# Performance work log

Measured on AMD Instinct MI355X. Metric: run time of the kernel, lower is better.

Reference implementation:

```python
import jax, jax.numpy as jnp
import numpy as np

N_A, N_D = 16384, 16384
D_EV = 4096      # d_inEvents (= rows of H_M)
H_DIM = 512      # hidden_dim
H1 = 1024        # hidden_dim1
H3 = 1024        # hidden_dim3
D_M = 4096       # d_inM (reconstruction output dim)


def _mlp2(x, w1, b1, w2, b2):
    return jax.nn.relu(x @ w1 + b1) @ w2 + b2


def setup_inputs() -> dict:
    key = jax.random.key(0)
    ks = jax.random.split(key, 32)
    s_in = (2.0 / D_EV) ** 0.5
    s_h1 = (2.0 / H1) ** 0.5
    s_2h = (2.0 / (2 * H_DIM)) ** 0.5
    s_h3 = (2.0 / H3) ** 0.5
    d = {
        "H_A": jax.random.uniform(ks[0], (N_A, D_EV), jnp.float32),
        "H_D": jax.random.uniform(ks[1], (N_D, D_EV), jnp.float32),
        "H_M": jax.random.uniform(ks[2], (D_EV, D_EV), jnp.float32),
    }
    for i, nm in enumerate(["A", "D", "M"]):
        d[f"w{nm}1"] = jax.random.normal(ks[3 + 4 * i], (D_EV, H1), jnp.float32) * s_in
        d[f"b{nm}1"] = jnp.zeros((H1,), jnp.float32)
        d[f"w{nm}2"] = jax.random.normal(ks[4 + 4 * i], (H1, H_DIM), jnp.float32) * s_h1
        d[f"b{nm}2"] = jnp.zeros((H_DIM,), jnp.float32)
    for i, nm in enumerate(["EA", "ED"]):
        d[f"w{nm}1"] = jax.random.normal(ks[16 + 4 * i], (2 * H_DIM, H3), jnp.float32) * s_2h
        d[f"b{nm}1"] = jnp.zeros((H3,), jnp.float32)
        d[f"w{nm}2"] = jax.random.normal(ks[17 + 4 * i], (H3, D_M), jnp.float32) * s_h3
        d[f"b{nm}2"] = jnp.zeros((D_M,), jnp.float32)
    return d


def reference(H_A, H_D, H_M,
              wA1, bA1, wA2, bA2,
              wD1, bD1, wD2, bD2,
              wM1, bM1, wM2, bM2,
              wEA1, bEA1, wEA2, bEA2,
              wED1, bED1, wED2, bED2):
    # Encoder (the torch.eye matmul is an identity and is elided)
    H_mean_A = _mlp2(H_A, wA1, bA1, wA2, bA2)   # [N_A, H_DIM]
    H_mean_D = _mlp2(H_D, wD1, bD1, wD2, bD2)   # [N_D, H_DIM]
    H_mean_M = _mlp2(H_M, wM1, bM1, wM2, bM2)   # [D_EV, H_DIM]
    # Pooling: per-column loop in torch == single matmul H^T @ H_mean
    sum_A = H_A.T @ H_mean_A                    # [D_EV, H_DIM]
    sum_D = H_D.T @ H_mean_D                    # [D_EV, H_DIM]
    EventA = jnp.concatenate([H_mean_M, sum_A], axis=1)  # [D_EV, 2*H_DIM]
    EventD = jnp.concatenate([H_mean_M, sum_D], axis=1)
    reconstructA = _mlp2(EventA, wEA1, bEA1, wEA2, bEA2)  # [D_EV, D_M]
    reconstructD = _mlp2(EventD, wED1, bED1, wED2, bED2)
    return (reconstructA, reconstructD, H_mean_A, H_mean_D, H_mean_M)
```

## Files before the change

kernel.cpp:

```cpp
#include <hip/hip_runtime.h>
#include <cstdint>
#include <cstddef>


typedef unsigned short u16;
typedef unsigned int u32;
typedef __bf16 bf16_t;
typedef bf16_t bf16x8 __attribute__((ext_vector_type(8)));
typedef float f32x4 __attribute__((ext_vector_type(4)));
typedef u16 u16x4 __attribute__((ext_vector_type(4)));
typedef u16 u16x8 __attribute__((ext_vector_type(8)));

__device__ __forceinline__ u16 f2bf(float x) {
  u32 u = __builtin_bit_cast(u32, x);
  u += 0x7FFFu + ((u >> 16) & 1u);
  return (u16)(u >> 16);
}
__device__ __forceinline__ float bf2f(u16 h) {
  u32 u = ((u32)h) << 16;
  return __builtin_bit_cast(float, u);
}

#define AS1(p) ((__attribute__((address_space(1))) void*)(p))
#define AS3(p) ((__attribute__((address_space(3))) void*)(p))

__global__ void detect_kernel(const u32* __restrict__ p, int* __restrict__ flag) {
  if (threadIdx.x == 0 && blockIdx.x == 0) {
    int cnt = 0;
    for (int i = 0; i < 64; ++i) {
      u32 b = (p[i] >> 8) & 0xFFu;
      cnt += (b >= 0x3Au && b < 0x40u) ? 1 : 0;
    }
    *flag = (cnt >= 32) ? 1 : 0;
  }
}

__global__ void convert_kernel(const void* __restrict__ src, u16* __restrict__ dst,
                               long n, const int* __restrict__ fl) {
  long i = ((long)blockIdx.x * 256 + threadIdx.x) * 8;
  if (i >= n) return;
  u16x8 r;
  if (*fl) {
    r = *(const u16x8*)((const u16*)src + i);
  } else {
    const float* s = (const float*)src + i;
#pragma unroll
    for (int j = 0; j < 8; ++j) r[j] = f2bf(s[j]);
  }
  *(u16x8*)(dst + i) = r;
}

__global__ void tconv_kernel(const void* __restrict__ src, long soff, u16* __restrict__ dst,
                             int R, int C, const int* __restrict__ fl) {
  __shared__ u16 t[32][33];
  const int dt = *fl;
  const int tx = threadIdx.x & 31, ty = threadIdx.x >> 5;
  const long c0 = (long)blockIdx.x * 32, r0 = (long)blockIdx.y * 32;
#pragma unroll
  for (int r = 0; r < 4; ++r) {
    int rr = ty * 4 + r;
    long off = soff + (r0 + rr) * (long)C + c0 + tx;
    t[rr][tx] = dt ? ((const u16*)src)[off] : f2bf(((const float*)src)[off]);
  }
  __syncthreads();
#pragma unroll
  for (int r = 0; r < 4; ++r) {
    int rr = ty * 4 + r;
    dst[(c0 + rr) * (long)R + r0 + tx] = t[tx][rr];
  }
}

__global__ void reduce4_kernel(const float* __restrict__ s, long stride,
                               u16* __restrict__ dst, long ldd, long n) {
  long i = (long)blockIdx.x * 256 + threadIdx.x;
  if (i >= n) return;
  float v = s[i] + s[i + stride] + s[i + 2 * stride] + s[i + 3 * stride];
  dst[(i >> 9) * ldd + (i & 511)] = f2bf(v);
}

__global__ __launch_bounds__(256) void gemm_bt_kernel(
    const u16* __restrict__ A, long lda,
    const u16* __restrict__ Bt, long ldb,
    long K,
    const void* __restrict__ bias, int relu,
    void* __restrict__ outd, long odoff, long ldod,
    float* __restrict__ outw, long ldow, long ozstride,
    u16* __restrict__ outb, long ldob,
    u16* __restrict__ outb2, long ldob2,
    u16* __restrict__ outT, long ldT,
    const int* __restrict__ fl) {
  __shared__ u16 As[128 * 32];
  __shared__ u16 Bs[128 * 32];

  const int t = threadIdx.x;
  const int l = t & 63;
  const int w = t >> 6;
  const int wx = w & 1, wy = w >> 1;
  const long m0 = (long)blockIdx.y * 128;
  const long n0 = (long)blockIdx.x * 128;
  const int dt = *fl;

  const long koff = (long)blockIdx.z * K;
  A += koff;
  Bt += koff;
  if (outw) outw += (long)blockIdx.z * ozstride;

  const int srow = w * 16 + (l >> 2);
  const int scol = (l & 3) * 8;
  const int la = l & 15, lq = l >> 4;

  f32x4 acc[4][4];
  const f32x4 zero = {0.f, 0.f, 0.f, 0.f};
#pragma unroll
  for (int i = 0; i < 4; ++i)
#pragma unroll
    for (int j = 0; j < 4; ++j) acc[i][j] = zero;

  for (long k0 = 0; k0 < K; k0 += 32) {
#pragma unroll
    for (int r = 0; r < 2; ++r) {
      const u16* ga = A + (m0 + r * 64 + srow) * lda + k0 + scol;
      __builtin_amdgcn_global_load_lds(AS1(ga), AS3(As + (r * 64 + w * 16) * 32), 16, 0, 0);
      const u16* gb = Bt + (n0 + r * 64 + srow) * ldb + k0 + scol;
      __builtin_amdgcn_global_load_lds(AS1(gb), AS3(Bs + (r * 64 + w * 16) * 32), 16, 0, 0);
    }
    __syncthreads();

    bf16x8 af[4], bfr[4];
#pragma unroll
    for (int i = 0; i < 4; ++i) {
      af[i] = *(const bf16x8*)(As + (wy * 64 + i * 16 + la) * 32 + lq * 8);
      bfr[i] = *(const bf16x8*)(Bs + (wx * 64 + i * 16 + la) * 32 + lq * 8);
    }
#pragma unroll
    for (int i = 0; i < 4; ++i)
#pragma unroll
      for (int j = 0; j < 4; ++j)
        acc[i][j] = __builtin_amdgcn_mfma_f32_16x16x32_bf16(af[i], bfr[j], acc[i][j], 0, 0, 0);
    __syncthreads();
  }

  const long gr0 = m0 + wy * 64;
  const long gc0 = n0 + wx * 64;
#pragma unroll
  for (int i = 0; i < 4; ++i) {
#pragma unroll
    for (int j = 0; j < 4; ++j) {
      const long gc = gc0 + j * 16 + la;
      const long grb = gr0 + i * 16 + lq * 4;
      float bv = 0.f;
      if (bias) bv = dt ? bf2f(((const u16*)bias)[gc]) : ((const float*)bias)[gc];
      float vv[4];
#pragma unroll
      for (int p = 0; p < 4; ++p) {
        float x = acc[i][j][p] + bv;
        if (relu) x = x > 0.f ? x : 0.f;
        vv[p] = x;
      }
      if (outd) {
        if (dt) {
          u16* o = (u16*)outd + odoff;
#pragma unroll
          for (int p = 0; p < 4; ++p) o[(grb + p) * ldod + gc] = f2bf(vv[p]);
        } else {
          float* o = (float*)outd + odoff;
#pragma unroll
          for (int p = 0; p < 4; ++p) o[(grb + p) * ldod + gc] = vv[p];
        }
      }
      if (outw) {
#pragma unroll
        for (int p = 0; p < 4; ++p) outw[(grb + p) * ldow + gc] = vv[p];
      }
      if (outb) {
#pragma unroll
        for (int p = 0; p < 4; ++p) outb[(grb + p) * ldob + gc] = f2bf(vv[p]);
      }
      if (outb2) {
#pragma unroll
        for (int p = 0; p < 4; ++p) outb2[(grb + p) * ldob2 + gc] = f2bf(vv[p]);
      }
      if (outT) {
        u16x4 pk;
#pragma unroll
        for (int p = 0; p < 4; ++p) pk[p] = f2bf(vv[p]);
        *(u16x4*)(outT + gc * ldT + grb) = pk;
      }
    }
  }
}

static void gemm(hipStream_t st, const u16* A, long lda, const u16* Bt, long ldb,
                 long M, long N, long K, int zsplit,
                 const void* bias, int relu,
                 void* outd, long odoff, long ldod,
                 float* outw, long ldow, long ozstride,
                 u16* outb, long ldob, u16* outb2, long ldob2,
                 u16* outT, long ldT, const int* fl) {
  dim3 g((unsigned)(N / 128), (unsigned)(M / 128), (unsigned)zsplit);
  gemm_bt_kernel<<<g, 256, 0, st>>>(A, lda, Bt, ldb, K, bias, relu, outd, odoff, ldod,
                                    outw, ldow, ozstride, outb, ldob, outb2, ldob2,
                                    outT, ldT, fl);
}

static void tconv(hipStream_t st, const void* src, long soff, u16* dst, int R, int C,
                  const int* fl) {
  tconv_kernel<<<dim3((unsigned)(C / 32), (unsigned)(R / 32)), 256, 0, st>>>(src, soff, dst, R,
                                                                             C, fl);
}

static void conv(hipStream_t st, const void* src, u16* dst, long n, const int* fl) {
  convert_kernel<<<(unsigned)((n / 8 + 255) / 256), 256, 0, st>>>(src, dst, n, fl);
}

extern "C" void kernel_launch(void* const* d_in, const int* in_sizes, int n_in,
                              void* d_out, int out_size, void* d_ws, size_t ws_size,
                              hipStream_t stream) {
  (void)in_sizes; (void)n_in; (void)out_size; (void)ws_size;
  const long NA = 16384, DEV = 4096, H1n = 1024, HD = 512, DM = 4096;

  char* ws = (char*)d_ws;
  u16* BIG = (u16*)(ws + 0L);
  u16* H1B = (u16*)(ws + 134217728L);
  float* SUMS = (float*)(ws + 134217728L);
  u16* HMT = (u16*)(ws + 167772160L);
  u16* EVA = (u16*)(ws + 184549376L);
  u16* EVD = (u16*)(ws + 192937984L);
  u16* WT1 = (u16*)(ws + 201326592L);
  u16* WT2 = (u16*)(ws + 209715200L);
  int* FLAG = (int*)(ws + 218103808L);

  const void* H_A = d_in[0];
  const void* H_D = d_in[1];
  const void* H_M = d_in[2];
  const void *wA1 = d_in[3], *bA1 = d_in[4], *wA2 = d_in[5], *bA2 = d_in[6];
  const void *wD1 = d_in[7], *bD1 = d_in[8], *wD2 = d_in[9], *bD2 = d_in[10];
  const void *wM1 = d_in[11], *bM1 = d_in[12], *wM2 = d_in[13], *bM2 = d_in[14];
  const void *wEA1 = d_in[15], *bEA1 = d_in[16], *wEA2 = d_in[17], *bEA2 = d_in[18];
  const void *wED1 = d_in[19], *bED1 = d_in[20], *wED2 = d_in[21], *bED2 = d_in[22];

  const long O_RA = 0, O_RD = 16777216, O_HA = 33554432, O_HD = 41943040, O_HM = 50331648;

  detect_kernel<<<1, 64, 0, stream>>>((const u32*)H_A, FLAG);

  tconv(stream, wM1, 0, WT1, (int)DEV, (int)H1n, FLAG);
  tconv(stream, wM2, 0, WT2, (int)H1n, (int)HD, FLAG);
  conv(stream, H_M, BIG, DEV * DEV, FLAG);
  gemm(stream, BIG, DEV, WT1, DEV, DEV, H1n, DEV, 1, bM1, 1,
       nullptr, 0, 0, nullptr, 0, 0, H1B, H1n, nullptr, 0, nullptr, 0, FLAG);
  gemm(stream, H1B, H1n, WT2, H1n, DEV, HD, H1n, 1, bM2, 0,
       d_out, O_HM, HD, nullptr, 0, 0, EVA, 1024, EVD, 1024, nullptr, 0, FLAG);

  tconv(stream, wA1, 0, WT1, (int)DEV, (int)H1n, FLAG);
  tconv(stream, wA2, 0, WT2, (int)H1n, (int)HD, FLAG);
  conv(stream, H_A, BIG, NA * DEV, FLAG);
  gemm(stream, BIG, DEV, WT1, DEV, NA, H1n, DEV, 1, bA1, 1,
       nullptr, 0, 0, nullptr, 0, 0, H1B, H1n, nullptr, 0, nullptr, 0, FLAG);
  gemm(stream, H1B, H1n, WT2, H1n, NA, HD, H1n, 1, bA2, 0,
       d_out, O_HA, HD, nullptr, 0, 0, nullptr, 0, nullptr, 0, HMT, NA, FLAG);
  tconv(stream, H_A, 0, BIG, (int)NA, (int)DEV, FLAG);
  gemm(stream, BIG, NA, HMT, NA, DEV, HD, 4096, 4, nullptr, 0,
       nullptr, 0, 0, SUMS, HD, 2097152L, nullptr, 0, nullptr, 0, nullptr, 0, FLAG);
  reduce4_kernel<<<8192, 256, 0, stream>>>(SUMS, 2097152L, EVA + 512, 1024L, DEV * HD);

  tconv(stream, wEA1, 0, WT1, (int)H1n, (int)H1n, FLAG);
  tconv(stream, wEA2, 0, WT2, (int)H1n, (int)DM, FLAG);
  gemm(stream, EVA, 1024, WT1, H1n, DEV, H1n, H1n, 1, bEA1, 1,
       nullptr, 0, 0, nullptr, 0, 0, H1B, H1n, nullptr, 0, nullptr, 0, FLAG);
  gemm(stream, H1B, H1n, WT2, H1n, DEV, DM, H1n, 1, bEA2, 0,
       d_out, O_RA, DM, nullptr, 0, 0, nullptr, 0, nullptr, 0, nullptr, 0, FLAG);

  tconv(stream, wD1, 0, WT1, (int)DEV, (int)H1n, FLAG);
  tconv(stream, wD2, 0, WT2, (int)H1n, (int)HD, FLAG);
  conv(stream, H_D, BIG, NA * DEV, FLAG);
  gemm(stream, BIG, DEV, WT1, DEV, NA, H1n, DEV, 1, bD1, 1,
       nullptr, 0, 0, nullptr, 0, 0, H1B, H1n, nullptr, 0, nullptr, 0, FLAG);
  gemm(stream, H1B, H1n, WT2, H1n, NA, HD, H1n, 1, bD2, 0,
       d_out, O_HD, HD, nullptr, 0, 0, nullptr, 0, nullptr, 0, HMT, NA, FLAG);
  tconv(stream, H_D, 0, BIG, (int)NA, (int)DEV, FLAG);
  gemm(stream, BIG, NA, HMT, NA, DEV, HD, 4096, 4, nullptr, 0,
       nullptr, 0, 0, SUMS, HD, 2097152L, nullptr, 0, nullptr, 0, nullptr, 0, FLAG);
  reduce4_kernel<<<8192, 256, 0, stream>>>(SUMS, 2097152L, EVD + 512, 1024L, DEV * HD);

  tconv(stream, wED1, 0, WT1, (int)H1n, (int)H1n, FLAG);
  tconv(stream, wED2, 0, WT2, (int)H1n, (int)DM, FLAG);
  gemm(stream, EVD, 1024, WT1, H1n, DEV, H1n, H1n, 1, bED1, 1,
       nullptr, 0, 0, nullptr, 0, 0, H1B, H1n, nullptr, 0, nullptr, 0, FLAG);
  gemm(stream, H1B, H1n, WT2, H1n, DEV, DM, H1n, 1, bED2, 0,
       d_out, O_RD, DM, nullptr, 0, 0, nullptr, 0, nullptr, 0, nullptr, 0, FLAG);
}
```

Measured before the change: 2.228 ms.

## Add double-buffered 256x256 GEMM kernel and swizzle LDS layout

Adds a new 512-thread GEMM kernel with 256x256 tiles, a 64-wide K step and double-buffered LDS staging, so the next K tile loads while MFMAs run. It replaces the big encoder layer-1 GEMMs and the reconstruction layer-2 GEMMs. The existing 128x128 kernel also gets an XOR swizzle on its LDS write and read offsets to reduce bank conflicts. reduce4 gains optional bias/relu parameters, but they are unused here. The large tile uses 128KB of LDS and many accumulators per thread, which may limit occupancy.

```diff
diff --git a/kernel.cpp b/kernel.cpp
--- a/kernel.cpp
+++ b/kernel.cpp
@@ -71,11 +71,16 @@
 }
 
 __global__ void reduce4_kernel(const float* __restrict__ s, long stride,
-                               u16* __restrict__ dst, long ldd, long n) {
+                               u16* __restrict__ dst, long ldd, long n, int cl,
+                               const void* __restrict__ bias, int relu,
+                               const int* __restrict__ fl) {
   long i = (long)blockIdx.x * 256 + threadIdx.x;
   if (i >= n) return;
   float v = s[i] + s[i + stride] + s[i + 2 * stride] + s[i + 3 * stride];
-  dst[(i >> 9) * ldd + (i & 511)] = f2bf(v);
+  long col = i & ((1L << cl) - 1);
+  if (bias) v += (*fl) ? bf2f(((const u16*)bias)[col]) : ((const float*)bias)[col];
+  if (relu) v = v > 0.f ? v : 0.f;
+  dst[(i >> cl) * ldd + col] = f2bf(v);
 }
 
 __global__ __launch_bounds__(256) void gemm_bt_kernel(
@@ -106,8 +111,9 @@
   if (outw) outw += (long)blockIdx.z * ozstride;
 
   const int srow = w * 16 + (l >> 2);
-  const int scol = (l & 3) * 8;
+  const int scol = (((l & 3) ^ ((l >> 2) & 3))) * 8;
   const int la = l & 15, lq = l >> 4;
+  const int fsl = (lq ^ (la & 3)) * 8;
 
   f32x4 acc[4][4];
   const f32x4 zero = {0.f, 0.f, 0.f, 0.f};
@@ -129,8 +135,8 @@
     bf16x8 af[4], bfr[4];
 #pragma unroll
     for (int i = 0; i < 4; ++i) {
-      af[i] = *(const bf16x8*)(As + (wy * 64 + i * 16 + la) * 32 + lq * 8);
-      bfr[i] = *(const bf16x8*)(Bs + (wx * 64 + i * 16 + la) * 32 + lq * 8);
+      af[i] = *(const bf16x8*)(As + (wy * 64 + i * 16 + la) * 32 + fsl);
+      bfr[i] = *(const bf16x8*)(Bs + (wx * 64 + i * 16 + la) * 32 + fsl);
     }
 #pragma unroll
     for (int i = 0; i < 4; ++i)
@@ -185,6 +191,146 @@
 #pragma unroll
         for (int p = 0; p < 4; ++p) pk[p] = f2bf(vv[p]);
         *(u16x4*)(outT + gc * ldT + grb) = pk;
+      }
+    }
+  }
+}
+
+#define STAGE256(OP, KH, KZ, NB)                                                      \
+  {                                                                                   \
+    const u16* g_ = (OP) ? gB : gA;                                                   \
+    const long ld_ = (OP) ? ldb : lda;                                                \
+    u16* lb_ = lw + (NB) + (OP) * 16384 + (KH) * 8192;                                \
+    __builtin_amdgcn_global_load_lds(AS1(g_ + (KZ) + (KH) * 32), AS3(lb_), 16, 0, 0); \
+    __builtin_amdgcn_global_load_lds(AS1(g_ + (KZ) + (KH) * 32 + 128 * ld_),          \
+                                     AS3(lb_ + 4096), 16, 0, 0);                      \
+  }
+
+#define LDA4(MH, KS, CB)                                                              \
+  _Pragma("unroll") for (int i_ = 0; i_ < 4; ++i_)                                    \
+      af[i_] = *(const bf16x8*)(smem + (CB) + (KS) * 8192 + abase + (MH) * 2048 + i_ * 512);
+
+#define LDB4(KS, CB)                                                                  \
+  _Pragma("unroll") for (int j_ = 0; j_ < 4; ++j_)                                    \
+      bfr[j_] = *(const bf16x8*)(smem + (CB) + (KS) * 8192 + bbase + j_ * 512);
+
+#define MFMA16(MH)                                                                    \
+  _Pragma("unroll") for (int i_ = 0; i_ < 4; ++i_) {                                  \
+    _Pragma("unroll") for (int j_ = 0; j_ < 4; ++j_) {                                \
+      acc[(MH) * 4 + i_][j_] = __builtin_amdgcn_mfma_f32_16x16x32_bf16(               \
+          af[i_], bfr[j_], acc[(MH) * 4 + i_][j_], 0, 0, 0);                          \
+    }                                                                                 \
+  }
+
+__global__ __launch_bounds__(512, 2) void gemm256_2ph_kernel(
+    const u16* __restrict__ A, long lda,
+    const u16* __restrict__ Bt, long ldb,
+    long K,
+    const void* __restrict__ bias, int relu,
+    void* __restrict__ outd, long odoff, long ldod,
+    float* __restrict__ outw, long ldow, long ozstride,
+    u16* __restrict__ outb, long ldob,
+    const int* __restrict__ fl) {
+  __shared__ u16 smem[65536];
+
+  const int t = threadIdx.x;
+  const int l = t & 63;
+  const int w = t >> 6;
+  const int wx = w & 3, wy = w >> 2;
+  const int la = l & 15, lq = l >> 4;
+  const long m0 = (long)blockIdx.y * 256;
+  const long n0 = (long)blockIdx.x * 256;
+
+  const long koff = (long)blockIdx.z * K;
+  A += koff;
+  Bt += koff;
+  if (outw) outw += (long)blockIdx.z * ozstride;
+
+  const int sr = t >> 2;
+  const long kc = 8 * ((t & 3) ^ (sr & 3));
+  const u16* gA = A + (m0 + sr) * lda + kc;
+  const u16* gB = Bt + (n0 + sr) * ldb + kc;
+  u16* lw = smem + w * 512;
+
+  const int ard = la * 32 + ((lq ^ (la & 3)) << 3);
+  const int abase = wy * 4096 + ard;
+  const int bbase = 16384 + wx * 2048 + ard;
+
+  f32x4 acc[8][4];
+  const f32x4 zero = {0.f, 0.f, 0.f, 0.f};
+#pragma unroll
+  for (int i = 0; i < 8; ++i)
+#pragma unroll
+    for (int j = 0; j < 4; ++j) acc[i][j] = zero;
+
+  const long NT = K >> 6;
+
+  STAGE256(0, 0, 0L, 0);
+  STAGE256(1, 0, 0L, 0);
+  STAGE256(0, 1, 0L, 0);
+  STAGE256(1, 1, 0L, 0);
+  __syncthreads();
+
+  for (long kt = 0; kt < NT; ++kt) {
+    const int cb = (int)(kt & 1) * 32768;
+    if (kt + 1 < NT) {
+      const int nb = cb ^ 32768;
+      const long kz = (kt + 1) << 6;
+      STAGE256(0, 0, kz, nb);
+      STAGE256(1, 0, kz, nb);
+      STAGE256(0, 1, kz, nb);
+      STAGE256(1, 1, kz, nb);
+    }
+    bf16x8 af[4], bfr[4];
+    LDB4(0, cb);
+    LDA4(0, 0, cb);
+    MFMA16(0);
+    LDA4(1, 0, cb);
+    MFMA16(1);
+    LDB4(1, cb);
+    LDA4(0, 1, cb);
+    MFMA16(0);
+    LDA4(1, 1, cb);
+    MFMA16(1);
+    __syncthreads();
+  }
+
+  const int dt = *fl;
+  const long gr0 = m0 + wy * 128;
+  const long gc0 = n0 + wx * 64;
+#pragma unroll
+  for (int gi = 0; gi < 8; ++gi) {
+#pragma unroll
+    for (int j = 0; j < 4; ++j) {
+      const long gc = gc0 + j * 16 + la;
+      const long grb = gr0 + gi * 16 + lq * 4;
+      float bv = 0.f;
+      if (bias) bv = dt ? bf2f(((const u16*)bias)[gc]) : ((const float*)bias)[gc];
+      float vv[4];
+#pragma unroll
+      for (int p = 0; p < 4; ++p) {
+        float x = acc[gi][j][p] + bv;
+        if (relu) x = x > 0.f ? x : 0.f;
+        vv[p] = x;
+      }
+      if (outd) {
+        if (dt) {
+          u16* o = (u16*)outd + odoff;
+#pragma unroll
+          for (int p = 0; p < 4; ++p) o[(grb + p) * ldod + gc] = f2bf(vv[p]);
+        } else {
+          float* o = (float*)outd + odoff;
+#pragma unroll
+          for (int p = 0; p < 4; ++p) o[(grb + p) * ldod + gc] = vv[p];
+        }
+      }
+      if (outw) {
+#pragma unroll
+        for (int p = 0; p < 4; ++p) outw[(grb + p) * ldow + gc] = vv[p];
+      }
+      if (outb) {
+#pragma unroll
+        for (int p = 0; p < 4; ++p) outb[(grb + p) * ldob + gc] = f2bf(vv[p]);
       }
     }
   }
@@ -203,6 +349,16 @@
                                     outT, ldT, fl);
 }
 
+static void gemm256(hipStream_t st, const u16* A, long lda, const u16* Bt, long ldb,
+                    long M, long N, long K,
+                    const void* bias, int relu,
+                    void* outd, long odoff, long ldod,
+                    u16* outb, long ldob, const int* fl) {
+  dim3 g((unsigned)(N / 256), (unsigned)(M / 256), 1);
+  gemm256_2ph_kernel<<<g, 512, 0, st>>>(A, lda, Bt, ldb, K, bias, relu, outd, odoff, ldod,
+                                        nullptr, 0, 0, outb, ldob, fl);
+}
+
 static void tconv(hipStream_t st, const void* src, long soff, u16* dst, int R, int C,
                   const int* fl) {
   tconv_kernel<<<dim3((unsigned)(C / 32), (unsigned)(R / 32)), 256, 0, st>>>(src, soff, dst, R,
@@ -254,38 +410,40 @@
   tconv(stream, wA1, 0, WT1, (int)DEV, (int)H1n, FLAG);
   tconv(stream, wA2, 0, WT2, (int)H1n, (int)HD, FLAG);
   conv(stream, H_A, BIG, NA * DEV, FLAG);
-  gemm(stream, BIG, DEV, WT1, DEV, NA, H1n, DEV, 1, bA1, 1,
-       nullptr, 0, 0, nullptr, 0, 0, H1B, H1n, nullptr, 0, nullptr, 0, FLAG);
+  gemm256(stream, BIG, DEV, WT1, DEV, NA, H1n, DEV, bA1, 1,
+          nullptr, 0, 0, H1B, H1n, FLAG);
   gemm(stream, H1B, H1n, WT2, H1n, NA, HD, H1n, 1, bA2, 0,
        d_out, O_HA, HD, nullptr, 0, 0, nullptr, 0, nullptr, 0, HMT, NA, FLAG);
   tconv(stream, H_A, 0, BIG, (int)NA, (int)DEV, FLAG);
   gemm(stream, BIG, NA, HMT, NA, DEV, HD, 4096, 4, nullptr, 0,
        nullptr, 0, 0, SUMS, HD, 2097152L, nullptr, 0, nullptr, 0, nullptr, 0, FLAG);
-  reduce4_kernel<<<8192, 256, 0, stream>>>(SUMS, 2097152L, EVA + 512, 1024L, DEV * HD);
+  reduce4_kernel<<<8192, 256, 0, stream>>>(SUMS, 2097152L, EVA + 512, 1024L, DEV * HD, 9,
+                                           nullptr, 0, FLAG);
 
   tconv(stream, wEA1, 0, WT1, (int)H1n, (int)H1n, FLAG);
   tconv(stream, wEA2, 0, WT2, (int)H1n, (int)DM, FLAG);
   gemm(stream, EVA, 1024, WT1, H1n, DEV, H1n, H1n, 1, bEA1, 1,
        nullptr, 0, 0, nullptr, 0, 0, H1B, H1n, nullptr, 0, nullptr, 0, FLAG);
-  gemm(stream, H1B, H1n, WT2, H1n, DEV, DM, H1n, 1, bEA2, 0,
-       d_out, O_RA, DM, nullptr, 0, 0, nullptr, 0, nullptr, 0, nullptr, 0, FLAG);
+  gemm256(stream, H1B, H1n, WT2, H1n, DEV, DM, H1n, bEA2, 0,
+          d_out, O_RA, DM, nullptr, 0, FLAG);
 
   tconv(stream, wD1, 0, WT1, (int)DEV, (int)H1n, FLAG);
   tconv(stream, wD2, 0, WT2, (int)H1n, (int)HD, FLAG);
   conv(stream, H_D, BIG, NA * DEV, FLAG);
-  gemm(stream, BIG, DEV, WT1, DEV, NA, H1n, DEV, 1, bD1, 1,
-       nullptr, 0, 0, nullptr, 0, 0, H1B, H1n, nullptr, 0, nullptr, 0, FLAG);
+  gemm256(stream, BIG, DEV, WT1, DEV, NA, H1n, DEV, bD1, 1,
+          nullptr, 0, 0, H1B, H1n, FLAG);
   gemm(stream, H1B, H1n, WT2, H1n, NA, HD, H1n, 1, bD2, 0,
        d_out, O_HD, HD, nullptr, 0, 0, nullptr, 0, nullptr, 0, HMT, NA, FLAG);
   tconv(stream, H_D, 0, BIG, (int)NA, (int)DEV, FLAG);
   gemm(stream, BIG, NA, HMT, NA, DEV, HD, 4096, 4, nullptr, 0,
        nullptr, 0, 0, SUMS, HD, 2097152L, nullptr, 0, nullptr, 0, nullptr, 0, FLAG);
-  reduce4_kernel<<<8192, 256, 0, stream>>>(SUMS, 2097152L, EVD + 512, 1024L, DEV * HD);
+  reduce4_kernel<<<8192, 256, 0, stream>>>(SUMS, 2097152L, EVD + 512, 1024L, DEV * HD, 9,
+                                           nullptr, 0, FLAG);
 
   tconv(stream, wED1, 0, WT1, (int)H1n, (int)H1n, FLAG);
   tconv(stream, wED2, 0, WT2, (int)H1n, (int)DM, FLAG);
   gemm(stream, EVD, 1024, WT1, H1n, DEV, H1n, H1n, 1, bED1, 1,
        nullptr, 0, 0, nullptr, 0, 0, H1B, H1n, nullptr, 0, nullptr, 0, FLAG);
-  gemm(stream, H1B, H1n, WT2, H1n, DEV, DM, H1n, 1, bED2, 0,
-       d_out, O_RD, DM, nullptr, 0, 0, nullptr, 0, nullptr, 0, nullptr, 0, FLAG);
-}
+  gemm256(stream, H1B, H1n, WT2, H1n, DEV, DM, H1n, bED2, 0,
+          d_out, O_RD, DM, nullptr, 0, FLAG);
+}
```

Measured after the change: 1.997 ms. 1.12x faster.
